# Optimization experiments

Measured on AMD Instinct MI355X. Metric: run time of the kernel, lower is better.

## Reference

```python
import jax, jax.numpy as jnp
import numpy as np

B, N, P, K, E = 4, 20000, 128, 128, 160000


def setup_inputs() -> dict:
    key = jax.random.key(0)
    ks = jax.random.split(key, 16)
    inv_p = 1.0 / np.sqrt(P)
    inv_3p = 1.0 / np.sqrt(3 * P)
    return {
        "x_in": jax.random.normal(ks[0], (B, N, P), jnp.float32),
        "vertex_areas": jax.random.uniform(ks[1], (B, N), jnp.float32, 1e-3, 1.0),
        "evals": jax.random.uniform(ks[2], (B, K), jnp.float32, 0.0, 10.0),
        "evecs": jax.random.normal(ks[3], (B, N, K), jnp.float32),
        "gradX_vals": jax.random.normal(ks[4], (B, E), jnp.float32),
        "gradY_vals": jax.random.normal(ks[5], (B, E), jnp.float32),
        "grad_rows": jax.random.randint(ks[6], (B, E), 0, N, jnp.int32),
        "grad_cols": jax.random.randint(ks[7], (B, E), 0, N, jnp.int32),
        # learned params
        "diffusion_times": jax.random.uniform(ks[8], (P,), jnp.float32, 1e-3, 0.1),
        "B_re": jax.random.normal(ks[9], (P, P), jnp.float32) * inv_p,
        "B_im": jax.random.normal(ks[10], (P, P), jnp.float32) * inv_p,
        "W1": jax.random.normal(ks[11], (P, 3 * P), jnp.float32) * inv_3p,
        "b1": jnp.zeros((P,), jnp.float32),
        "W2": jax.random.normal(ks[12], (P, P), jnp.float32) * inv_p,
        "b2": jnp.zeros((P,), jnp.float32),
        "W3": jax.random.normal(ks[13], (P, P), jnp.float32) * inv_p,
        "b3": jnp.zeros((P,), jnp.float32),
    }


def _spmm(rows, cols, vals, x):
    # sparse (n,n) @ dense (n,p) via COO gather/scatter
    return jax.ops.segment_sum(vals[:, None] * x[cols], rows, num_segments=x.shape[0])


def reference(x_in, vertex_areas, evals, evecs, gradX_vals, gradY_vals,
              grad_rows, grad_cols, diffusion_times, B_re, B_im,
              W1, b1, W2, b2, W3, b3):
    # SpectralDiffusion: project -> spectral heat scaling -> unproject
    times = jnp.clip(diffusion_times, 1e-8)                       # (P,)
    x_spec = jnp.einsum('bnk,bnp->bkp', evecs, x_in * vertex_areas[..., None])
    scale = jnp.exp(-evals[..., None] * times[None, None, :])     # (B,K,P)
    x_diffuse = jnp.einsum('bnk,bkp->bnp', evecs, scale * x_spec)  # (B,N,P)

    # sparse gradient halves
    gx = jax.vmap(_spmm)(grad_rows, grad_cols, gradX_vals, x_diffuse)  # (B,N,P)
    gy = jax.vmap(_spmm)(grad_rows, grad_cols, gradY_vals, x_diffuse)

    # SpatialGradient: tanh(re*B_re(re) + im*B_im(im))
    x_grad_features = jnp.tanh(gx * (gx @ B_re.T) + gy * (gy @ B_im.T))

    # MiniMLP on concatenated features (dropout inactive in eval)
    h = jnp.concatenate([x_in, x_diffuse, x_grad_features], axis=-1)  # (B,N,3P)
    h = jax.nn.relu(h @ W1.T + b1)
    h = jax.nn.relu(h @ W2.T + b2)
    h = h @ W3.T + b3
    return h + x_in
```

## Files before the change

kernel.cpp:

```cpp
#include <hip/hip_runtime.h>
#include <hip/hip_bf16.h>
#include <cstddef>

#define B_ 4
#define N_ 20000
#define P_ 128
#define K_ 128
#define E_ 160000

constexpr int NCH_S = 79;
constexpr int NSCB  = 79;

typedef __attribute__((ext_vector_type(8))) short short8;
typedef __attribute__((ext_vector_type(4))) float f32x4;

__device__ __forceinline__ unsigned pk2(float x, float y) {
  __hip_bfloat162 h = __float22bfloat162_rn(make_float2(x, y));
  union { __hip_bfloat162 h; unsigned u; } c; c.h = h; return c.u;
}
__device__ __forceinline__ float bf2f(short s) {
  union { unsigned u; float f; } c; c.u = ((unsigned)(unsigned short)s) << 16; return c.f;
}

__global__ __launch_bounds__(256)
void k_prep(const float* __restrict__ ev, const float* __restrict__ xin,
            const float* __restrict__ areas,
            __hip_bfloat16* __restrict__ evT, __hip_bfloat16* __restrict__ xT)
{
  const int tn = blockIdx.x, half = blockIdx.y & 1, mat = blockIdx.y >> 1;
  const int b = blockIdx.z, t = threadIdx.x;
  const int n0 = tn * 64, c0 = half * 64;
  __shared__ float ld[64][65];
  const float* src = (mat ? xin : ev) + (size_t)b * N_ * 128;
  const float* ab  = areas + (size_t)b * N_;
#pragma unroll
  for (int i = 0; i < 4; ++i) {
    int gid = t + i * 256;
    int r = gid >> 4, c4 = (gid & 15) << 2;
    int n = n0 + r;
    float4 v = make_float4(0.f, 0.f, 0.f, 0.f);
    if (n < N_) {
      v = *(const float4*)(src + (size_t)n * 128 + c0 + c4);
      if (mat == 0) { float ar = ab[n]; v.x *= ar; v.y *= ar; v.z *= ar; v.w *= ar; }
    }
    ld[r][c4] = v.x; ld[r][c4+1] = v.y; ld[r][c4+2] = v.z; ld[r][c4+3] = v.w;
  }
  __syncthreads();
  __hip_bfloat16* dst = (mat ? xT : evT) + (size_t)b * 128 * N_;
#pragma unroll
  for (int i = 0; i < 4; ++i) {
    int gid = t + i * 256;
    int cr = gid >> 4, nq = (gid & 15) << 2;
    int n = n0 + nq;
    if (n + 4 <= N_) {
      uint2 u;
      u.x = pk2(ld[nq][cr],   ld[nq+1][cr]);
      u.y = pk2(ld[nq+2][cr], ld[nq+3][cr]);
      *(uint2*)(dst + (size_t)(c0 + cr) * N_ + n) = u;
    }
  }
}

__global__ __launch_bounds__(256)
void k_wprep(const float* __restrict__ Bre, const float* __restrict__ Bim,
             uint4* __restrict__ WfRe, uint4* __restrict__ WfIm)
{
  int fid = blockIdx.x * 256 + threadIdx.x;
  if (fid >= 2048) return;
  int gg = fid >> 7, rr = fid & 127;
  const float* s0 = Bre + rr * 128 + gg * 8;
  const float* s1 = Bim + rr * 128 + gg * 8;
  float4 a0 = *(const float4*)s0, a1 = *(const float4*)(s0 + 4);
  uint4 u; u.x = pk2(a0.x, a0.y); u.y = pk2(a0.z, a0.w);
  u.z = pk2(a1.x, a1.y); u.w = pk2(a1.z, a1.w);
  WfRe[fid] = u;
  float4 b0 = *(const float4*)s1, b1 = *(const float4*)(s1 + 4);
  uint4 v; v.x = pk2(b0.x, b0.y); v.y = pk2(b0.z, b0.w);
  v.z = pk2(b1.x, b1.y); v.w = pk2(b1.z, b1.w);
  WfIm[fid] = v;
}

__device__ __forceinline__ void stg64(uint4* __restrict__ Ls,
                                      const __hip_bfloat16* __restrict__ G,
                                      int n0, int t)
{
#pragma unroll
  for (int i = 0; i < 2; ++i) {
    int gid = t + i * 512;
    int r = gid >> 3, kg = gid & 7;
    int n = n0 + kg * 8;
    uint4 u = make_uint4(0u, 0u, 0u, 0u);
    if (n < N_) u = *(const uint4*)(G + (size_t)r * N_ + n);
    Ls[r * 8 + (kg ^ (r & 7))] = u;
  }
}

__global__ __launch_bounds__(512)
void k_spec_mm(const __hip_bfloat16* __restrict__ evT,
               const __hip_bfloat16* __restrict__ xT,
               float* __restrict__ part)
{
  const int c = blockIdx.x, b = blockIdx.y, t = threadIdx.x;
  const int l = t & 63, wid = t >> 6;
  const int wr = wid >> 2, wc = wid & 3;
  const int lr = l & 15, lg = l >> 4;
  __shared__ uint4 AsB[1024];
  __shared__ uint4 WsB[1024];
  f32x4 acc[4][2];
#pragma unroll
  for (int m = 0; m < 4; ++m)
#pragma unroll
    for (int n = 0; n < 2; ++n) acc[m][n] = (f32x4)0.f;

  const __hip_bfloat16* eb = evT + (size_t)b * 128 * N_;
  const __hip_bfloat16* xb = xT  + (size_t)b * 128 * N_;

  for (int s = 0; s < 4; ++s) {
    int n0 = c * 256 + s * 64;
    __syncthreads();
    stg64(AsB, eb, n0, t);
    stg64(WsB, xb, n0, t);
    __syncthreads();
    const short8* Ap = (const short8*)AsB;
    const short8* Wp = (const short8*)WsB;
#pragma unroll
    for (int kk = 0; kk < 2; ++kk) {
      int gg = kk * 4 + lg;
      short8 a[4], w[2];
#pragma unroll
      for (int m = 0; m < 4; ++m) { int rr = wr*64 + m*16 + lr; a[m] = Ap[rr*8 + (gg ^ (rr & 7))]; }
#pragma unroll
      for (int n = 0; n < 2; ++n) { int rr = wc*32 + n*16 + lr; w[n] = Wp[rr*8 + (gg ^ (rr & 7))]; }
#pragma unroll
      for (int m = 0; m < 4; ++m)
#pragma unroll
        for (int n = 0; n < 2; ++n)
          acc[m][n] = __builtin_amdgcn_mfma_f32_16x16x32_bf16(a[m], w[n], acc[m][n], 0, 0, 0);
    }
  }

  float* po = part + ((size_t)(b * NCH_S + c) << 14);
#pragma unroll
  for (int m = 0; m < 4; ++m)
#pragma unroll
    for (int r = 0; r < 4; ++r) {
      int row = wr*64 + m*16 + lg*4 + r;
#pragma unroll
      for (int n = 0; n < 2; ++n) {
        int col = wc*32 + n*16 + lr;
        po[row * 128 + col] = acc[m][n][r];
      }
    }
}

__global__ __launch_bounds__(256)
void k_spec_reduce(const float* __restrict__ partial, const float* __restrict__ evals,
                   const float* __restrict__ times, float* __restrict__ sspecT)
{
  int idx = blockIdx.x * 256 + threadIdx.x;
  int b = idx >> 14;
  int kp = idx & 16383;
  int k = kp >> 7, p = kp & 127;
  float s = 0.f;
  const float* pb = partial + (size_t)b * NCH_S * (K_*P_) + kp;
  for (int c = 0; c < NCH_S; ++c) s += pb[(size_t)c * (K_*P_)];
  float tt = times[p]; tt = tt < 1e-8f ? 1e-8f : tt;
  float sc = __expf(-evals[b*K_ + k] * tt);
  sspecT[((size_t)b*P_ + p) * K_ + k] = s * sc;
}

__device__ __forceinline__ void stg_f32(uint4* __restrict__ Ls, const float* __restrict__ G,
                                        int ld, int nrows, int t)
{
#pragma unroll
  for (int i = 0; i < 4; ++i) {
    int gid = t + i * 512;
    int r = gid >> 4, kg = gid & 15;
    float4 v0 = make_float4(0.f,0.f,0.f,0.f), v1 = v0;
    if (r < nrows) {
      const float* p = G + (size_t)r * ld + kg * 8;
      v0 = *(const float4*)p;
      v1 = *(const float4*)(p + 4);
    }
    uint4 u;
    u.x = pk2(v0.x, v0.y); u.y = pk2(v0.z, v0.w);
    u.z = pk2(v1.x, v1.y); u.w = pk2(v1.z, v1.w);
    Ls[r * 16 + (kg ^ (r & 7))] = u;
  }
}

__device__ __forceinline__ void stg_bf(uint4* __restrict__ Ls,
                                       const __hip_bfloat16* __restrict__ G,
                                       int ld, int nrows, int t)
{
#pragma unroll
  for (int i = 0; i < 4; ++i) {
    int gid = t + i * 512;
    int r = gid >> 4, kg = gid & 15;
    uint4 u = make_uint4(0u,0u,0u,0u);
    if (r < nrows) u = *(const uint4*)(G + (size_t)r * ld + kg * 8);
    Ls[r * 16 + (kg ^ (r & 7))] = u;
  }
}

__device__ __forceinline__ void mfma_chunk(const uint4* AsB, const uint4* WsB,
                                           int wr, int wc, int lr, int lg,
                                           f32x4 acc[4][2])
{
  const short8* Ap = (const short8*)AsB;
  const short8* Wp = (const short8*)WsB;
#pragma unroll
  for (int kk = 0; kk < 4; ++kk) {
    int gg = kk * 4 + lg;
    short8 a[4], w[2];
#pragma unroll
    for (int m = 0; m < 4; ++m) {
      int rr = wr*64 + m*16 + lr;
      a[m] = Ap[rr*16 + (gg ^ (rr & 7))];
    }
#pragma unroll
    for (int n = 0; n < 2; ++n) {
      int rr = wc*32 + n*16 + lr;
      w[n] = Wp[rr*16 + (gg ^ (rr & 7))];
    }
#pragma unroll
    for (int m = 0; m < 4; ++m)
#pragma unroll
      for (int n = 0; n < 2; ++n)
        acc[m][n] = __builtin_amdgcn_mfma_f32_16x16x32_bf16(a[m], w[n], acc[m][n], 0, 0, 0);
  }
}

template<int MODE>
__global__ __launch_bounds__(512)
void k_rowgemm(const void* __restrict__ A0, const void* __restrict__ A1,
               const void* __restrict__ A2, int abf,
               const float* __restrict__ W, int ldw, int wbs, int nchunk,
               const float* __restrict__ bias, const float* __restrict__ resid,
               void* __restrict__ C)
{
  const int b = blockIdx.y, r0 = blockIdx.x * 128, t = threadIdx.x;
  const int l = t & 63, wid = t >> 6;
  const int wr = wid >> 2, wc = wid & 3;
  const int lr = l & 15, lg = l >> 4;
  __shared__ uint4 AsB[2048];
  __shared__ uint4 WsB[2048];
  f32x4 acc[4][2];
#pragma unroll
  for (int m = 0; m < 4; ++m)
#pragma unroll
    for (int n = 0; n < 2; ++n) acc[m][n] = (f32x4)0.f;

  const float* Wb = W + (size_t)b * wbs;
  const int nrows = min(128, N_ - r0);
  const size_t aoff = (size_t)b * N_ * 128 + (size_t)r0 * 128;

  for (int kc = 0; kc < nchunk; ++kc) {
    const void* Av = (kc == 0 ? A0 : (kc == 1 ? A1 : A2));
    __syncthreads();
    if ((abf >> kc) & 1) stg_bf(AsB, (const __hip_bfloat16*)Av + aoff, 128, nrows, t);
    else                 stg_f32(AsB, (const float*)Av + aoff, 128, nrows, t);
    stg_f32(WsB, Wb + kc * 128, ldw, 128, t);
    __syncthreads();
    mfma_chunk(AsB, WsB, wr, wc, lr, lg, acc);
  }

  const size_t cb = (size_t)b * N_ * 128;
#pragma unroll
  for (int m = 0; m < 4; ++m) {
    int rowt = wr*64 + m*16 + lg*4;
#pragma unroll
    for (int r = 0; r < 4; ++r) {
      int row = r0 + rowt + r;
      if (row >= N_) continue;
#pragma unroll
      for (int n = 0; n < 2; ++n) {
        int col = wc*32 + n*16 + lr;
        float v = acc[m][n][r];
        if (MODE == 1 || MODE == 2) v = fmaxf(v + bias[col], 0.f);
        if (MODE == 3) {
          v += bias[col] + resid[cb + (size_t)row*128 + col];
          ((float*)C)[cb + (size_t)row*128 + col] = v;
        } else {
          ((__hip_bfloat16*)C)[cb + (size_t)row*128 + col] = __float2bfloat16(v);
        }
      }
    }
  }
}

__device__ __forceinline__ void stg64r(uint4* __restrict__ Ls,
                                       const __hip_bfloat16* __restrict__ G,
                                       int nrows, int t)
{
#pragma unroll
  for (int i = 0; i < 4; ++i) {
    int gid = t + i * 256;
    int r = gid >> 4, kg = gid & 15;
    uint4 u = make_uint4(0u,0u,0u,0u);
    if (r < nrows) u = *(const uint4*)(G + (size_t)r * 128 + kg * 8);
    Ls[r * 16 + (kg ^ (r & 7))] = u;
  }
}

__device__ __forceinline__ void mfma_pass64(const uint4* As, const uint4* __restrict__ Wf,
                                            int wc, int lr, int lg, f32x4 acc[4][2])
{
  const short8* Ap = (const short8*)As;
  const short8* Wp = (const short8*)Wf;
#pragma unroll
  for (int kk = 0; kk < 4; ++kk) {
    int gg = kk * 4 + lg;
    short8 a[4], w[2];
#pragma unroll
    for (int m = 0; m < 4; ++m) { int rr = m*16 + lr; a[m] = Ap[rr*16 + (gg ^ (rr & 7))]; }
#pragma unroll
    for (int n = 0; n < 2; ++n) { int rr = wc*32 + n*16 + lr; w[n] = Wp[(gg << 7) + rr]; }
#pragma unroll
    for (int m = 0; m < 4; ++m)
#pragma unroll
      for (int n = 0; n < 2; ++n)
        acc[m][n] = __builtin_amdgcn_mfma_f32_16x16x32_bf16(a[m], w[n], acc[m][n], 0, 0, 0);
  }
}

__global__ __launch_bounds__(256)
void k_grad(const uint4* __restrict__ WfRe, const uint4* __restrict__ WfIm,
            __hip_bfloat16* __restrict__ gx, const __hip_bfloat16* __restrict__ gy)
{
  const int b = blockIdx.y, r0 = blockIdx.x * 64, t = threadIdx.x;
  const int l = t & 63, wc = t >> 6;
  const int lr = l & 15, lg = l >> 4;
  __shared__ uint4 As[1024];
  f32x4 acc1[4][2], acc2[4][2];
#pragma unroll
  for (int m = 0; m < 4; ++m)
#pragma unroll
    for (int n = 0; n < 2; ++n) { acc1[m][n] = (f32x4)0.f; acc2[m][n] = (f32x4)0.f; }

  __hip_bfloat16*       gxb = gx + (size_t)b * N_ * P_;
  const __hip_bfloat16* gyb = gy + (size_t)b * N_ * P_;
  const int nrows = min(64, N_ - r0);

  stg64r(As, gxb + (size_t)r0 * 128, nrows, t);
  __syncthreads();
  mfma_pass64(As, WfRe, wc, lr, lg, acc1);
  __syncthreads();
  stg64r(As, gyb + (size_t)r0 * 128, nrows, t);
#pragma unroll
  for (int m = 0; m < 4; ++m)
#pragma unroll
    for (int r = 0; r < 4; ++r) {
      int row = r0 + m*16 + lg*4 + r;
      if (row >= N_) continue;
#pragma unroll
      for (int n = 0; n < 2; ++n) {
        int col = wc*32 + n*16 + lr;
        acc1[m][n][r] *= bf2f(*(const short*)(gxb + (size_t)row*128 + col));
      }
    }
  __syncthreads();
  mfma_pass64(As, WfIm, wc, lr, lg, acc2);

#pragma unroll
  for (int m = 0; m < 4; ++m)
#pragma unroll
    for (int r = 0; r < 4; ++r) {
      int row = r0 + m*16 + lg*4 + r;
      if (row >= N_) continue;
#pragma unroll
      for (int n = 0; n < 2; ++n) {
        int col = wc*32 + n*16 + lr;
        float g2 = bf2f(*(const short*)(gyb + (size_t)row*128 + col));
        float s = acc1[m][n][r] + g2 * acc2[m][n][r];
        s = fminf(fmaxf(s, -15.f), 15.f);
        float e = __expf(2.f * s);
        gxb[(size_t)row*128 + col] = __float2bfloat16((e - 1.f) / (e + 1.f));
      }
    }
}

__global__ void k_count(const int* __restrict__ rows, int* __restrict__ cnt)
{
  int b = blockIdx.y;
  int e = blockIdx.x * 256 + threadIdx.x;
  if (e < E_) atomicAdd(&cnt[b*N_ + rows[(size_t)b*E_ + e]], 1);
}

__global__ __launch_bounds__(256)
void k_scan_blk(const int* __restrict__ cnt, int* __restrict__ off,
                int* __restrict__ bsum)
{
  const int c = blockIdx.x, b = blockIdx.y, t = threadIdx.x;
  const int lane = t & 63, wid = t >> 6;
  __shared__ int wt[4];
  int i = c * 256 + t;
  int v = (i < N_) ? cnt[b*N_ + i] : 0;
  int x = v;
#pragma unroll
  for (int ofs = 1; ofs < 64; ofs <<= 1) {
    int y = __shfl_up(x, ofs, 64);
    if (lane >= ofs) x += y;
  }
  if (lane == 63) wt[wid] = x;
  __syncthreads();
  int wofs = 0;
  for (int wj = 0; wj < wid; ++wj) wofs += wt[wj];
  if (i < N_) off[b*(N_+1) + i] = wofs + x - v;
  if (t == 255) bsum[b*128 + c] = wofs + x;
}

__global__ __launch_bounds__(64)
void k_scan_top(int* __restrict__ bsum, int* __restrict__ off)
{
  const int b = blockIdx.x, t = threadIdx.x;
  int running = 0;
  for (int base = 0; base < 128; base += 64) {
    int i = base + t;
    int v = (i < NSCB) ? bsum[b*128 + i] : 0;
    int x = v;
#pragma unroll
    for (int ofs = 1; ofs < 64; ofs <<= 1) {
      int y = __shfl_up(x, ofs, 64);
      if (t >= ofs) x += y;
    }
    if (i < 128) bsum[b*128 + i] = running + x - v;
    running += __shfl(x, 63, 64);
  }
  if (t == 0) off[b*(N_+1) + N_] = running;
}

__global__ __launch_bounds__(256)
void k_scan_add(const int* __restrict__ bsum, int* __restrict__ off,
                int* __restrict__ pos)
{
  const int c = blockIdx.x, b = blockIdx.y;
  int i = c * 256 + (int)threadIdx.x;
  if (i < N_) {
    int o = off[b*(N_+1) + i] + bsum[b*128 + c];
    off[b*(N_+1) + i] = o;
    pos[b*N_ + i] = o;
  }
}

__global__ void k_fill(const int* __restrict__ rows, const int* __restrict__ cols,
                       const float* __restrict__ vx, const float* __restrict__ vy,
                       int* __restrict__ pos, int* __restrict__ pcid,
                       float* __restrict__ pvx, float* __restrict__ pvy)
{
  int b = blockIdx.y;
  int e = blockIdx.x * 256 + threadIdx.x;
  if (e < E_) {
    size_t be = (size_t)b*E_ + e;
    int r = rows[be];
    int p = atomicAdd(&pos[b*N_ + r], 1);
    if (p >= 0 && p < E_) {
      size_t bp = (size_t)b*E_ + p;
      pcid[bp] = cols[be];
      pvx[bp]  = vx[be];
      pvy[bp]  = vy[be];
    }
  }
}

__global__ __launch_bounds__(256)
void k_gather(const __hip_bfloat16* __restrict__ xd, const int* __restrict__ pcid,
              const float* __restrict__ pvx, const float* __restrict__ pvy,
              const int* __restrict__ off,
              __hip_bfloat16* __restrict__ gx, __hip_bfloat16* __restrict__ gy)
{
  const int b = blockIdx.y;
  const int row = (blockIdx.x * 256 + threadIdx.x) >> 6;
  const int lane = threadIdx.x & 63;
  if (row >= N_) return;
  const int s = off[b*(N_+1) + row], e = off[b*(N_+1) + row + 1];
  float ax0 = 0.f, ax1 = 0.f, ay0 = 0.f, ay1 = 0.f;
  const __hip_bfloat16* xdb = xd + (size_t)b * N_ * P_;
  const size_t bE = (size_t)b * E_;

  for (int base = s; base < e; base += 64) {
    const int cnt = min(64, e - base);
    int cid = 0; float wx = 0.f, wy = 0.f;
    if (lane < cnt) {
      cid = pcid[bE + base + lane];
      wx  = pvx[bE + base + lane];
      wy  = pvy[bE + base + lane];
    }
    for (int i = 0; i < cnt; ++i) {
      int   c  = __shfl(cid, i, 64);
      float fx = __shfl(wx,  i, 64);
      float fy = __shfl(wy,  i, 64);
      unsigned v = *(const unsigned*)(xdb + (size_t)c * P_ + lane*2);
      float x0 = bf2f((short)(v & 0xffff));
      float x1 = bf2f((short)(v >> 16));
      ax0 = fmaf(fx, x0, ax0); ax1 = fmaf(fx, x1, ax1);
      ay0 = fmaf(fy, x0, ay0); ay1 = fmaf(fy, x1, ay1);
    }
  }
  size_t o = (size_t)b * N_ * P_ + (size_t)row * P_ + lane*2;
  *(unsigned*)(gx + o) = pk2(ax0, ax1);
  *(unsigned*)(gy + o) = pk2(ay0, ay1);
}

extern "C" void kernel_launch(void* const* d_in, const int* in_sizes, int n_in,
                              void* d_out, int out_size, void* d_ws, size_t ws_size,
                              hipStream_t stream)
{
  const float* x_in  = (const float*)d_in[0];
  const float* areas = (const float*)d_in[1];
  const float* evals = (const float*)d_in[2];
  const float* evecs = (const float*)d_in[3];
  const float* gXv   = (const float*)d_in[4];
  const float* gYv   = (const float*)d_in[5];
  const int*   grows = (const int*)d_in[6];
  const int*   gcols = (const int*)d_in[7];
  const float* times = (const float*)d_in[8];
  const float* Bre   = (const float*)d_in[9];
  const float* Bim   = (const float*)d_in[10];
  const float* W1    = (const float*)d_in[11];
  const float* b1    = (const float*)d_in[12];
  const float* W2    = (const float*)d_in[13];
  const float* b2    = (const float*)d_in[14];
  const float* W3    = (const float*)d_in[15];
  const float* b3    = (const float*)d_in[16];

  float* ws = (float*)d_ws;
  __hip_bfloat16* xd_bf = (__hip_bfloat16*)ws;
  float*          part  = ws + 6000000;
  __hip_bfloat16* gx_bf = (__hip_bfloat16*)(ws + 12000000);
  __hip_bfloat16* gy_bf = (__hip_bfloat16*)(ws + 18000000);
  __hip_bfloat16* evT   = gx_bf;
  __hip_bfloat16* xT    = gy_bf;

  int*   ipos   = (int*)(ws + 24000000);
  int*   ioff   = ipos + B_*N_;
  int*   pcid   = ioff + B_*(N_+1);
  float* pvx    = (float*)(pcid + (size_t)B_*E_);
  float* pvy    = pvx + (size_t)B_*E_;
  float* sspecT = pvy + (size_t)B_*E_;
  uint4* WfRe   = (uint4*)(sspecT + (size_t)B_*P_*K_);
  uint4* WfIm   = WfRe + 2048;
  int*   bsum   = (int*)(WfIm + 2048);
  float* out    = (float*)d_out;

  const int GB = (N_ + 127) / 128;
  const int TN = (N_ + 63) / 64;

  k_prep<<<dim3(TN, 4, B_), 256, 0, stream>>>(evecs, x_in, areas, evT, xT);
  k_wprep<<<dim3(8), 256, 0, stream>>>(Bre, Bim, WfRe, WfIm);
  k_spec_mm<<<dim3(NCH_S, B_), 512, 0, stream>>>(evT, xT, part);
  k_spec_reduce<<<dim3(B_*K_*P_/256), 256, 0, stream>>>(part, evals, times, sspecT);
  k_rowgemm<0><<<dim3(GB, B_), 512, 0, stream>>>(evecs, nullptr, nullptr, 0, sspecT,
                                                 128, K_*P_, 1, nullptr, nullptr, xd_bf);
  hipMemsetAsync(ipos, 0, (size_t)B_*N_*sizeof(int), stream);
  k_count<<<dim3(E_/256, B_), 256, 0, stream>>>(grows, ipos);
  k_scan_blk<<<dim3(NSCB, B_), 256, 0, stream>>>(ipos, ioff, bsum);
  k_scan_top<<<dim3(B_), 64, 0, stream>>>(bsum, ioff);
  k_scan_add<<<dim3(NSCB, B_), 256, 0, stream>>>(bsum, ioff, ipos);
  k_fill<<<dim3(E_/256, B_), 256, 0, stream>>>(grows, gcols, gXv, gYv, ipos,
                                               pcid, pvx, pvy);
  k_gather<<<dim3(N_/4, B_), 256, 0, stream>>>(xd_bf, pcid, pvx, pvy, ioff,
                                               gx_bf, gy_bf);
  k_grad<<<dim3(TN, B_), 256, 0, stream>>>(WfRe, WfIm, gx_bf, gy_bf);
  k_rowgemm<1><<<dim3(GB, B_), 512, 0, stream>>>(x_in, xd_bf, gx_bf, 0b110, W1,
                                                 384, 0, 3, b1, nullptr, gy_bf);
  k_rowgemm<2><<<dim3(GB, B_), 512, 0, stream>>>(gy_bf, nullptr, nullptr, 1, W2,
                                                 128, 0, 1, b2, nullptr, gx_bf);
  k_rowgemm<3><<<dim3(GB, B_), 512, 0, stream>>>(gx_bf, nullptr, nullptr, 1, W3,
                                                 128, 0, 1, b3, x_in, out);
}
```

Before: 284.6 us.

## Pack CSR edge records into uint4 and process two edges per wavefront

After: 286.1 us. About the same (+0.5%).

```diff
diff --git a/kernel.cpp b/kernel.cpp
--- a/kernel.cpp
+++ b/kernel.cpp
@@ -445,8 +445,7 @@
 
 __global__ void k_fill(const int* __restrict__ rows, const int* __restrict__ cols,
                        const float* __restrict__ vx, const float* __restrict__ vy,
-                       int* __restrict__ pos, int* __restrict__ pcid,
-                       float* __restrict__ pvx, float* __restrict__ pvy)
+                       int* __restrict__ pos, uint4* __restrict__ prec)
 {
   int b = blockIdx.y;
   int e = blockIdx.x * 256 + threadIdx.x;
@@ -455,51 +454,59 @@
     int r = rows[be];
     int p = atomicAdd(&pos[b*N_ + r], 1);
     if (p >= 0 && p < E_) {
-      size_t bp = (size_t)b*E_ + p;
-      pcid[bp] = cols[be];
-      pvx[bp]  = vx[be];
-      pvy[bp]  = vy[be];
-    }
-  }
-}
-
-__global__ __launch_bounds__(256)
-void k_gather(const __hip_bfloat16* __restrict__ xd, const int* __restrict__ pcid,
-              const float* __restrict__ pvx, const float* __restrict__ pvy,
+      uint4 rec;
+      rec.x = (unsigned)cols[be];
+      rec.y = __float_as_uint(vx[be]);
+      rec.z = __float_as_uint(vy[be]);
+      rec.w = 0u;
+      prec[(size_t)b*E_ + p] = rec;
+    }
+  }
+}
+
+__global__ __launch_bounds__(256)
+void k_gather(const __hip_bfloat16* __restrict__ xd, const uint4* __restrict__ prec,
               const int* __restrict__ off,
               __hip_bfloat16* __restrict__ gx, __hip_bfloat16* __restrict__ gy)
 {
   const int b = blockIdx.y;
   const int row = (blockIdx.x * 256 + threadIdx.x) >> 6;
   const int lane = threadIdx.x & 63;
+  const int half = lane >> 5, cl = lane & 31;
   if (row >= N_) return;
   const int s = off[b*(N_+1) + row], e = off[b*(N_+1) + row + 1];
-  float ax0 = 0.f, ax1 = 0.f, ay0 = 0.f, ay1 = 0.f;
+  float ax0 = 0.f, ax1 = 0.f, ax2 = 0.f, ax3 = 0.f;
+  float ay0 = 0.f, ay1 = 0.f, ay2 = 0.f, ay3 = 0.f;
   const __hip_bfloat16* xdb = xd + (size_t)b * N_ * P_;
-  const size_t bE = (size_t)b * E_;
-
-  for (int base = s; base < e; base += 64) {
-    const int cnt = min(64, e - base);
-    int cid = 0; float wx = 0.f, wy = 0.f;
-    if (lane < cnt) {
-      cid = pcid[bE + base + lane];
-      wx  = pvx[bE + base + lane];
-      wy  = pvy[bE + base + lane];
-    }
-    for (int i = 0; i < cnt; ++i) {
-      int   c  = __shfl(cid, i, 64);
-      float fx = __shfl(wx,  i, 64);
-      float fy = __shfl(wy,  i, 64);
-      unsigned v = *(const unsigned*)(xdb + (size_t)c * P_ + lane*2);
-      float x0 = bf2f((short)(v & 0xffff));
-      float x1 = bf2f((short)(v >> 16));
-      ax0 = fmaf(fx, x0, ax0); ax1 = fmaf(fx, x1, ax1);
-      ay0 = fmaf(fy, x0, ay0); ay1 = fmaf(fy, x1, ay1);
-    }
-  }
-  size_t o = (size_t)b * N_ * P_ + (size_t)row * P_ + lane*2;
-  *(unsigned*)(gx + o) = pk2(ax0, ax1);
-  *(unsigned*)(gy + o) = pk2(ay0, ay1);
+  const uint4* pb = prec + (size_t)b * E_;
+
+  for (int i = s; i < e; i += 2) {
+    int idx = i + half;
+    bool valid = idx < e;
+    uint4 rec = pb[valid ? idx : (e - 1)];
+    float fx = valid ? __uint_as_float(rec.y) : 0.f;
+    float fy = valid ? __uint_as_float(rec.z) : 0.f;
+    uint2 v = *(const uint2*)(xdb + (size_t)rec.x * P_ + cl * 4);
+    float x0 = __uint_as_float(v.x << 16);
+    float x1 = __uint_as_float(v.x & 0xffff0000u);
+    float x2 = __uint_as_float(v.y << 16);
+    float x3 = __uint_as_float(v.y & 0xffff0000u);
+    ax0 = fmaf(fx, x0, ax0); ax1 = fmaf(fx, x1, ax1);
+    ax2 = fmaf(fx, x2, ax2); ax3 = fmaf(fx, x3, ax3);
+    ay0 = fmaf(fy, x0, ay0); ay1 = fmaf(fy, x1, ay1);
+    ay2 = fmaf(fy, x2, ay2); ay3 = fmaf(fy, x3, ay3);
+  }
+  ax0 += __shfl_xor(ax0, 32, 64); ax1 += __shfl_xor(ax1, 32, 64);
+  ax2 += __shfl_xor(ax2, 32, 64); ax3 += __shfl_xor(ax3, 32, 64);
+  ay0 += __shfl_xor(ay0, 32, 64); ay1 += __shfl_xor(ay1, 32, 64);
+  ay2 += __shfl_xor(ay2, 32, 64); ay3 += __shfl_xor(ay3, 32, 64);
+  if (half == 0) {
+    size_t o = (size_t)b * N_ * P_ + (size_t)row * P_ + cl * 4;
+    uint2 ux; ux.x = pk2(ax0, ax1); ux.y = pk2(ax2, ax3);
+    uint2 uy; uy.x = pk2(ay0, ay1); uy.y = pk2(ay2, ay3);
+    *(uint2*)(gx + o) = ux;
+    *(uint2*)(gy + o) = uy;
+  }
 }
 
 extern "C" void kernel_launch(void* const* d_in, const int* in_sizes, int n_in,
@@ -532,13 +539,11 @@
   __hip_bfloat16* evT   = gx_bf;
   __hip_bfloat16* xT    = gy_bf;
 
-  int*   ipos   = (int*)(ws + 24000000);
+  uint4* prec   = (uint4*)(ws + 24000000);
+  int*   ipos   = (int*)(ws + 26560000);
   int*   ioff   = ipos + B_*N_;
-  int*   pcid   = ioff + B_*(N_+1);
-  float* pvx    = (float*)(pcid + (size_t)B_*E_);
-  float* pvy    = pvx + (size_t)B_*E_;
-  float* sspecT = pvy + (size_t)B_*E_;
-  uint4* WfRe   = (uint4*)(sspecT + (size_t)B_*P_*K_);
+  float* sspecT = ws + 26750000;
+  uint4* WfRe   = (uint4*)(ws + 26816000);
   uint4* WfIm   = WfRe + 2048;
   int*   bsum   = (int*)(WfIm + 2048);
   float* out    = (float*)d_out;
@@ -557,10 +562,8 @@
   k_scan_blk<<<dim3(NSCB, B_), 256, 0, stream>>>(ipos, ioff, bsum);
   k_scan_top<<<dim3(B_), 64, 0, stream>>>(bsum, ioff);
   k_scan_add<<<dim3(NSCB, B_), 256, 0, stream>>>(bsum, ioff, ipos);
-  k_fill<<<dim3(E_/256, B_), 256, 0, stream>>>(grows, gcols, gXv, gYv, ipos,
-                                               pcid, pvx, pvy);
-  k_gather<<<dim3(N_/4, B_), 256, 0, stream>>>(xd_bf, pcid, pvx, pvy, ioff,
-                                               gx_bf, gy_bf);
+  k_fill<<<dim3(E_/256, B_), 256, 0, stream>>>(grows, gcols, gXv, gYv, ipos, prec);
+  k_gather<<<dim3(N_/4, B_), 256, 0, stream>>>(xd_bf, prec, ioff, gx_bf, gy_bf);
   k_grad<<<dim3(TN, B_), 256, 0, stream>>>(WfRe, WfIm, gx_bf, gy_bf);
   k_rowgemm<1><<<dim3(GB, B_), 512, 0, stream>>>(x_in, xd_bf, gx_bf, 0b110, W1,
                                                  384, 0, 3, b1, nullptr, gy_bf);
```
